# Kernel tuning notes

Measured on AMD Instinct MI355X. Metric: run time of the kernel, lower is better.

## Reference

```python
import jax, jax.numpy as jnp
import numpy as np

B, S, D, F_INT = 8, 1024, 1024, 4096
N_EDGES = 262144
NUM_REL = 2
LN_EPS = 1e-6


def setup_inputs() -> dict:
    key = jax.random.key(0)
    ks = jax.random.split(key, 10)
    N = B * S
    glorot_w = float(np.sqrt(6.0 / (D + F_INT)))
    glorot_r = float(np.sqrt(6.0 / (D + F_INT)))
    return {
        "hidden_states": jax.random.normal(ks[0], (B, S, D), dtype=jnp.float32),
        "weight": jax.random.uniform(ks[1], (NUM_REL, D, F_INT), jnp.float32, -glorot_w, glorot_w),
        "root": jax.random.uniform(ks[2], (D, F_INT), jnp.float32, -glorot_r, glorot_r),
        "bias": jnp.zeros((F_INT,), jnp.float32),
        "wo": jax.random.normal(ks[3], (F_INT, D), dtype=jnp.float32) * 0.02,
        "ln_gamma": jnp.ones((D,), jnp.float32),
        "ln_beta": jnp.zeros((D,), jnp.float32),
        "edge_index": jax.random.randint(ks[4], (2, N_EDGES), 0, N, dtype=jnp.int32),
        "edge_type": jax.random.randint(ks[5], (N_EDGES,), 0, NUM_REL, dtype=jnp.int32),
    }


def reference(hidden_states, weight, root, bias, wo, ln_gamma, ln_beta, edge_index, edge_type):
    Bz, Sq, Dm = hidden_states.shape
    N = Bz * Sq
    # LayerNorm
    mu = hidden_states.mean(-1, keepdims=True)
    var = jnp.mean((hidden_states - mu) ** 2, axis=-1, keepdims=True)
    norm_x = (hidden_states - mu) * jax.lax.rsqrt(var + LN_EPS) * ln_gamma + ln_beta
    x = norm_x.reshape(N, Dm)  # [N, D] node features

    src, dst = edge_index[0], edge_index[1]
    out = jnp.zeros((N, weight.shape[2]), dtype=x.dtype)
    # RGCNConv: per-relation masked gather -> scatter-mean -> matmul
    for r in range(NUM_REL):
        mask = (edge_type == r)
        msg = jnp.where(mask[:, None], x[src], 0.0)          # [E, D]
        agg = jax.ops.segment_sum(msg, dst, num_segments=N)  # [N, D]
        cnt = jax.ops.segment_sum(mask.astype(x.dtype), dst, num_segments=N)
        h = agg / jnp.maximum(cnt, 1.0)[:, None]             # mean aggr (0 if no edges)
        out = out + h @ weight[r]
    out = out + x @ root + bias
    # relu -> wo -> residual (dropout = identity at eval)
    out = jax.nn.relu(out) @ wo
    return hidden_states + out.reshape(Bz, Sq, Dm)
```

## Files before the change

### kernel.cpp

```cpp
#include <hip/hip_runtime.h>


typedef unsigned short u16;
typedef unsigned int   u32;
typedef __attribute__((ext_vector_type(8))) short bf16x8;
typedef __attribute__((ext_vector_type(4))) float f32x4;
typedef __attribute__((ext_vector_type(2))) float f32x2;

#define E_NUM  262144
#define NNODE  8192
#define NBKT   (2 * NNODE)
#define DDIM   1024
#define FDIM   4096
#define KCAT   3072
#define LN_EPS 1e-6f

struct alignas(8) u16x4 { u16 x, y, z, w; };

__device__ __forceinline__ u16 f2bf(float f) {
  u32 u = __float_as_uint(f);
  u32 r = u + 0x7fffu + ((u >> 16) & 1u);
  return (u16)(r >> 16);
}
__device__ __forceinline__ float bf2f(u16 h) {
  return __uint_as_float(((u32)h) << 16);
}

__device__ __forceinline__ u32 enc_fp8_1(float f) {
  u32 u = __float_as_uint(f);
  u32 s = u >> 31;
  u32 mag = u & 0x7fffffffu;
  mag = mag + 0x7ffffu + ((mag >> 20) & 1u);
  if (mag > 0x43e00000u) mag = 0x43e00000u;
  u32 e = mag >> 23;
  return (e <= 120u) ? 0u
                     : ((s << 7) | ((e - 120u) << 3) | ((mag >> 20) & 7u));
}

__device__ __forceinline__ u32 pack4_fp8(float a, float b, float c, float d) {
#if __has_builtin(__builtin_amdgcn_cvt_pk_fp8_f32)
  int v = 0;
  v = __builtin_amdgcn_cvt_pk_fp8_f32(a, b, v, false);
  v = __builtin_amdgcn_cvt_pk_fp8_f32(c, d, v, true);
  return (u32)v;
#else
  return enc_fp8_1(a) | (enc_fp8_1(b) << 8) | (enc_fp8_1(c) << 16) |
         (enc_fp8_1(d) << 24);
#endif
}

__device__ __forceinline__ float dec_fp8_1(u32 b) {
  u32 e = (b >> 3) & 15u;
  u32 f = ((b & 0x80u) << 24) | ((e + 120u) << 23) | ((b & 7u) << 20);
  return e ? __uint_as_float(f) : 0.0f;
}

__device__ __forceinline__ void acc4_fp8(float* a, u32 q) {
#if __has_builtin(__builtin_amdgcn_cvt_pk_f32_fp8)
  f32x2 p0 = __builtin_amdgcn_cvt_pk_f32_fp8((int)q, false);
  f32x2 p1 = __builtin_amdgcn_cvt_pk_f32_fp8((int)q, true);
  a[0] += p0.x; a[1] += p0.y; a[2] += p1.x; a[3] += p1.y;
#else
  a[0] += dec_fp8_1(q);       a[1] += dec_fp8_1(q >> 8);
  a[2] += dec_fp8_1(q >> 16); a[3] += dec_fp8_1(q >> 24);
#endif
}

#define GLD16(gp, lp)                                              \
  __builtin_amdgcn_global_load_lds(                                \
      (__attribute__((address_space(1))) u32*)(gp),                \
      (__attribute__((address_space(3))) u32*)(lp), 16, 0, 0)

__global__ void ln_kernel(const float* __restrict__ hs,
                          const float* __restrict__ gamma,
                          const float* __restrict__ beta,
                          u16* __restrict__ hcat,
                          u32* __restrict__ xq) {
  const int row = blockIdx.x;
  const int tid = threadIdx.x;
  const float4 v = ((const float4*)(hs + (size_t)row * DDIM))[tid];

  __shared__ float r1[256], r2[256];
  r1[tid] = v.x + v.y + v.z + v.w;
  r2[tid] = v.x * v.x + v.y * v.y + v.z * v.z + v.w * v.w;
  __syncthreads();
  for (int st = 128; st > 0; st >>= 1) {
    if (tid < st) { r1[tid] += r1[tid + st]; r2[tid] += r2[tid + st]; }
    __syncthreads();
  }
  const float mean = r1[0] * (1.0f / DDIM);
  const float var  = r2[0] * (1.0f / DDIM) - mean * mean;
  const float rs   = rsqrtf(var + LN_EPS);

  const int base = tid * 4;
  const float4 g = *(const float4*)(gamma + base);
  const float4 b = *(const float4*)(beta + base);
  const float o0 = (v.x - mean) * rs * g.x + b.x;
  const float o1 = (v.y - mean) * rs * g.y + b.y;
  const float o2 = (v.z - mean) * rs * g.z + b.z;
  const float o3 = (v.w - mean) * rs * g.w + b.w;
  u16x4 o;
  o.x = f2bf(o0); o.y = f2bf(o1); o.z = f2bf(o2); o.w = f2bf(o3);
  *(u16x4*)(hcat + (size_t)row * KCAT + 2048 + base) = o;
  xq[row * 256 + tid] = pack4_fp8(o0, o1, o2, o3);
}

__global__ void cvt_transpose(const float* __restrict__ srcA,
                              const float* __restrict__ srcB,
                              int splitK, int K, int N,
                              u16* __restrict__ dst) {
  __shared__ float tile[32][33];
  const int n0 = blockIdx.x * 32, k0 = blockIdx.y * 32;
  const int tx = threadIdx.x, ty = threadIdx.y;
  for (int i = ty; i < 32; i += 8) {
    const int k = k0 + i;
    const float v = (k < splitK) ? srcA[(size_t)k * N + n0 + tx]
                                 : srcB[(size_t)(k - splitK) * N + n0 + tx];
    tile[i][tx] = v;
  }
  __syncthreads();
  for (int i = ty; i < 32; i += 8) {
    dst[(size_t)(n0 + i) * K + k0 + tx] = f2bf(tile[tx][i]);
  }
}

__global__ void count_kernel(const int* __restrict__ edge_index,
                             const int* __restrict__ edge_type,
                             int* __restrict__ cnt) {
  const int e = blockIdx.x * 256 + threadIdx.x;
  const int d = edge_index[E_NUM + e];
  const int r = edge_type[e];
  atomicAdd(&cnt[r * NNODE + d], 1);
}

__global__ __launch_bounds__(1024) void scan_kernel(const int* __restrict__ cnt,
                                                    int* __restrict__ off,
                                                    int* __restrict__ cursor) {
  __shared__ int partial[1024];
  const int tid  = threadIdx.x;
  const int base = tid * 16;
  int local[16];
  int s = 0;
#pragma unroll
  for (int i = 0; i < 16; ++i) { local[i] = s; s += cnt[base + i]; }
  partial[tid] = s;
  __syncthreads();
  for (int st = 1; st < 1024; st <<= 1) {
    const int v = (tid >= st) ? partial[tid - st] : 0;
    __syncthreads();
    partial[tid] += v;
    __syncthreads();
  }
  const int pre = (tid == 0) ? 0 : partial[tid - 1];
#pragma unroll
  for (int i = 0; i < 16; ++i) {
    const int o = pre + local[i];
    off[base + i]    = o;
    cursor[base + i] = o;
  }
}

__global__ void fill_kernel(const int* __restrict__ edge_index,
                            const int* __restrict__ edge_type,
                            int* __restrict__ cursor,
                            int* __restrict__ bucket_src) {
  const int e = blockIdx.x * 256 + threadIdx.x;
  const int s = edge_index[e];
  const int d = edge_index[E_NUM + e];
  const int r = edge_type[e];
  const int pos = atomicAdd(&cursor[r * NNODE + d], 1);
  bucket_src[pos] = s;
}

__global__ __launch_bounds__(256) void aggregate_kernel(
    const int* __restrict__ cnt, const int* __restrict__ off,
    const int* __restrict__ bucket_src, const u32* __restrict__ xq,
    u16* __restrict__ hcat) {
  const int b    = blockIdx.x;
  const int r    = b >> 13;
  const int node = b & (NNODE - 1);
  const int tid  = threadIdx.x;
  const int g    = tid >> 6;
  const int c    = tid & 63;
  const int n     = cnt[b];
  const int start = off[b];

  __shared__ int   ids[256];
  __shared__ float red[3 * 1024];
  float a[16] = {};

  for (int c0 = 0; c0 < n; c0 += 256) {
    const int m = min(n - c0, 256);
    __syncthreads();
    if (tid < m) ids[tid] = bucket_src[start + c0 + tid];
    __syncthreads();
    int j = g;
    for (; j + 4 < m; j += 8) {
      const int s0 = ids[j], s1 = ids[j + 4];
      const uint4 x0 = *(const uint4*)(xq + s0 * 256 + c * 4);
      const uint4 x1 = *(const uint4*)(xq + s1 * 256 + c * 4);
      acc4_fp8(a + 0,  x0.x); acc4_fp8(a + 4,  x0.y);
      acc4_fp8(a + 8,  x0.z); acc4_fp8(a + 12, x0.w);
      acc4_fp8(a + 0,  x1.x); acc4_fp8(a + 4,  x1.y);
      acc4_fp8(a + 8,  x1.z); acc4_fp8(a + 12, x1.w);
    }
    for (; j < m; j += 4) {
      const int s0 = ids[j];
      const uint4 x0 = *(const uint4*)(xq + s0 * 256 + c * 4);
      acc4_fp8(a + 0,  x0.x); acc4_fp8(a + 4,  x0.y);
      acc4_fp8(a + 8,  x0.z); acc4_fp8(a + 12, x0.w);
    }
  }

  if (g != 0) {
    float* d = red + (g - 1) * 1024 + c * 16;
#pragma unroll
    for (int i = 0; i < 4; ++i)
      *(float4*)(d + i * 4) = make_float4(a[i*4+0], a[i*4+1], a[i*4+2], a[i*4+3]);
  }
  __syncthreads();
  if (g == 0) {
#pragma unroll
    for (int k = 0; k < 3; ++k) {
      const float* d = red + k * 1024 + c * 16;
#pragma unroll
      for (int i = 0; i < 16; ++i) a[i] += d[i];
    }
    const float inv = 1.0f / fmaxf((float)n, 1.0f);
    uint4 o0, o1;
    o0.x = (u32)f2bf(a[0] * inv)  | ((u32)f2bf(a[1] * inv)  << 16);
    o0.y = (u32)f2bf(a[2] * inv)  | ((u32)f2bf(a[3] * inv)  << 16);
    o0.z = (u32)f2bf(a[4] * inv)  | ((u32)f2bf(a[5] * inv)  << 16);
    o0.w = (u32)f2bf(a[6] * inv)  | ((u32)f2bf(a[7] * inv)  << 16);
    o1.x = (u32)f2bf(a[8] * inv)  | ((u32)f2bf(a[9] * inv)  << 16);
    o1.y = (u32)f2bf(a[10] * inv) | ((u32)f2bf(a[11] * inv) << 16);
    o1.z = (u32)f2bf(a[12] * inv) | ((u32)f2bf(a[13] * inv) << 16);
    o1.w = (u32)f2bf(a[14] * inv) | ((u32)f2bf(a[15] * inv) << 16);
    u16* dp = hcat + (size_t)node * KCAT + (size_t)r * DDIM + c * 16;
    *(uint4*)(dp)     = o0;
    *(uint4*)(dp + 8) = o1;
  }
}


#define MF16(a, b, c) __builtin_amdgcn_mfma_f32_16x16x32_bf16(a, b, c, 0, 0, 0)

#define STAGE_A(t, p, b)                                                   \
  { GLD16(gA0 + (size_t)(t) * 64 + (size_t)(p) * KP,                       \
          &sA[b][(p) * 8192 + lofs0]);                                     \
    GLD16(gA1 + (size_t)(t) * 64 + (size_t)(p) * KP,                       \
          &sA[b][(p) * 8192 + lofs1]); }

#define STAGE_B(t, p, b)                                                   \
  { GLD16(gB0 + (size_t)(t) * 64 + (size_t)(p) * KP,                       \
          &sB[b][(p) * 8192 + lofs0]);                                     \
    GLD16(gB1 + (size_t)(t) * 64 + (size_t)(p) * KP,                       \
          &sB[b][(p) * 8192 + lofs1]); }

#define BVLOAD(b)                                                          \
  { const bf16x8* pB_ = (const bf16x8*)sB[b];                              \
    bv[0][0] = pB_[brow80 + sega0]; bv[0][1] = pB_[brow80 + sega1];        \
    bv[1][0] = pB_[brow81 + sega0]; bv[1][1] = pB_[brow81 + sega1];        \
    bv[2][0] = pB_[brow82 + sega0]; bv[2][1] = pB_[brow82 + sega1];        \
    bv[3][0] = pB_[brow83 + sega0]; bv[3][1] = pB_[brow83 + sega1]; }

#define NOWAIT ((void)0)
#define NOSTAGE ((void)0)
#define VM4 asm volatile("s_waitcnt vmcnt(4)" ::: "memory")
#define VM0 asm volatile("s_waitcnt vmcnt(0)" ::: "memory")

#define PHASE(Q, BUFI, STAGE, ENDW)                                        \
  { const bf16x8* pA_ = (const bf16x8*)sA[BUFI];                           \
    bf16x8 a00 = pA_[arow8[2 * (Q)] + sega0];                              \
    bf16x8 a01 = pA_[arow8[2 * (Q)] + sega1];                              \
    bf16x8 a10 = pA_[arow8[2 * (Q) + 1] + sega0];                          \
    bf16x8 a11 = pA_[arow8[2 * (Q) + 1] + sega1];                          \
    STAGE;                                                                 \
    __builtin_amdgcn_s_barrier();                                          \
    asm volatile("s_waitcnt lgkmcnt(0)" ::: "memory");                     \
    __builtin_amdgcn_s_setprio(1);                                         \
    _Pragma("unroll")                                                      \
    for (int ni = 0; ni < 4; ++ni) {                                       \
      acc[2 * (Q)][ni]     = MF16(a00, bv[ni][0], acc[2 * (Q)][ni]);       \
      acc[2 * (Q)][ni]     = MF16(a01, bv[ni][1], acc[2 * (Q)][ni]);       \
      acc[2 * (Q) + 1][ni] = MF16(a10, bv[ni][0], acc[2 * (Q) + 1][ni]);   \
      acc[2 * (Q) + 1][ni] = MF16(a11, bv[ni][1], acc[2 * (Q) + 1][ni]);   \
    }                                                                      \
    __builtin_amdgcn_s_setprio(0);                                         \
    ENDW;                                                                  \
    __builtin_amdgcn_s_barrier(); }

__global__ __launch_bounds__(512) void gemm1_kernel(
    const u16* __restrict__ A, const u16* __restrict__ Bt,
    const float* __restrict__ bias, u16* __restrict__ obf) {
  const int K = KCAT, N = FDIM;
  const int NT = K / 64;
  const size_t KP = (size_t)128 * K;
  __shared__ __align__(16) u16 sA[2][16384];
  __shared__ __align__(16) u16 sB[2][16384];

  const int tid  = threadIdx.x;
  const int lane = tid & 63;
  const int wave = tid >> 6;
  const int wr = wave >> 2, wc = wave & 3;
  const int lr = lane & 15, quad = lane >> 4;

  const int bid = blockIdx.x;
  const int swz = (bid & 7) * 64 + (bid >> 3);
  const int bm = (swz >> 4) * 256;
  const int bn = (swz & 15) * 256;

  int lofs0, lofs1;
  const u16 *gA0, *gA1, *gB0, *gB1;
  {
    const int s0 = tid,       r0 = s0 >> 3, g0 = (s0 & 7) ^ (r0 & 7);
    const int s1 = tid + 512, r1 = s1 >> 3, g1 = (s1 & 7) ^ (r1 & 7);
    gA0 = A  + (size_t)(bm + r0) * K + g0 * 8;
    gA1 = A  + (size_t)(bm + r1) * K + g1 * 8;
    gB0 = Bt + (size_t)(bn + r0) * K + g0 * 8;
    gB1 = Bt + (size_t)(bn + r1) * K + g1 * 8;
    lofs0 = s0 * 8; lofs1 = s1 * 8;
  }

  int arow8[8];
#pragma unroll
  for (int mi = 0; mi < 8; ++mi) arow8[mi] = (wr * 128 + mi * 16 + lr) * 8;
  const int brow80 = (wc * 64 +  0 + lr) * 8;
  const int brow81 = (wc * 64 + 16 + lr) * 8;
  const int brow82 = (wc * 64 + 32 + lr) * 8;
  const int brow83 = (wc * 64 + 48 + lr) * 8;
  const int sega0 = quad ^ (lr & 7);
  const int sega1 = (4 + quad) ^ (lr & 7);

  f32x4 acc[8][4] = {};
  bf16x8 bv[4][2];

  STAGE_B(0, 0, 0) STAGE_B(0, 1, 0)
  STAGE_A(0, 0, 0) STAGE_A(0, 1, 0)
  STAGE_B(1, 0, 1) STAGE_B(1, 1, 1)
  asm volatile("s_waitcnt vmcnt(4)" ::: "memory");
  __builtin_amdgcn_s_barrier();

  for (int tt = 0; tt < NT - 2; tt += 2) {
    PHASE(0, 0, BVLOAD(0); STAGE_A(tt + 1, 0, 1), NOWAIT)
    PHASE(1, 0, STAGE_A(tt + 1, 1, 1), NOWAIT)
    PHASE(2, 0, STAGE_B(tt + 2, 0, 0), NOWAIT)
    PHASE(3, 0, STAGE_B(tt + 2, 1, 0), VM4)
    PHASE(0, 1, BVLOAD(1); STAGE_A(tt + 2, 0, 0), NOWAIT)
    PHASE(1, 1, STAGE_A(tt + 2, 1, 0), NOWAIT)
    PHASE(2, 1, STAGE_B(tt + 3, 0, 1), NOWAIT)
    PHASE(3, 1, STAGE_B(tt + 3, 1, 1), VM4)
  }
  PHASE(0, 0, BVLOAD(0); STAGE_A(NT - 1, 0, 1), NOWAIT)
  PHASE(1, 0, STAGE_A(NT - 1, 1, 1), NOWAIT)
  PHASE(2, 0, NOSTAGE, NOWAIT)
  PHASE(3, 0, NOSTAGE, VM0)
  PHASE(0, 1, BVLOAD(1), NOWAIT)
  PHASE(1, 1, NOSTAGE, NOWAIT)
  PHASE(2, 1, NOSTAGE, NOWAIT)
  PHASE(3, 1, NOSTAGE, NOWAIT)

#pragma unroll
  for (int mi = 0; mi < 8; ++mi) {
#pragma unroll
    for (int ni = 0; ni < 4; ++ni) {
      const int col  = bn + wc * 64 + ni * 16 + lr;
      const int row0 = bm + wr * 128 + mi * 16 + quad * 4;
      const float bb = bias[col];
#pragma unroll
      for (int r = 0; r < 4; ++r) {
        float v = acc[mi][ni][r] + bb;
        v = fmaxf(v, 0.0f);
        obf[(size_t)(row0 + r) * N + col] = f2bf(v);
      }
    }
  }
}

__global__ __launch_bounds__(256) void gemm2_kernel(
    const u16* __restrict__ A, const u16* __restrict__ Bt,
    const float* __restrict__ resid, float* __restrict__ out) {
  const int K = FDIM, N = DDIM;
  __shared__ __align__(16) u16 sA[64 * 64];
  __shared__ __align__(16) u16 sB[128 * 64];
  const int tid  = threadIdx.x;
  const int lane = tid & 63;
  const int wave = tid >> 6;
  const int bm = blockIdx.x * 64;
  const int bn = blockIdx.y * 128;
  const int wm = (wave >> 1) * 32;
  const int wn = (wave & 1) * 64;
  const int lr   = lane & 15;
  const int quad = lane >> 4;

  f32x4 acc[2][4] = {};

  const u16* gA[2]; u16* lA[2];
#pragma unroll
  for (int i = 0; i < 2; ++i) {
    const int s   = tid + 256 * i;
    const int row = s >> 3;
    const int seg = (s & 7) ^ (row & 7);
    gA[i] = A + (size_t)(bm + row) * K + seg * 8;
    lA[i] = sA + s * 8;
  }
  const u16* gB[4]; u16* lB[4];
#pragma unroll
  for (int i = 0; i < 4; ++i) {
    const int s   = tid + 256 * i;
    const int row = s >> 3;
    const int seg = (s & 7) ^ (row & 7);
    gB[i] = Bt + (size_t)(bn + row) * K + seg * 8;
    lB[i] = sB + s * 8;
  }

  int ai[2][2], bi[4][2];
#pragma unroll
  for (int h = 0; h < 2; ++h) {
#pragma unroll
    for (int mi = 0; mi < 2; ++mi) {
      const int ra = wm + mi * 16 + lr;
      ai[mi][h] = ra * 8 + ((h * 4 + quad) ^ (ra & 7));
    }
#pragma unroll
    for (int ni = 0; ni < 4; ++ni) {
      const int rb = wn + ni * 16 + lr;
      bi[ni][h] = rb * 8 + ((h * 4 + quad) ^ (rb & 7));
    }
  }

  for (int k0 = 0; k0 < K; k0 += 64) {
#pragma unroll
    for (int i = 0; i < 2; ++i) GLD16(gA[i] + k0, lA[i]);
#pragma unroll
    for (int i = 0; i < 4; ++i) GLD16(gB[i] + k0, lB[i]);
    __syncthreads();

    const bf16x8* pA = (const bf16x8*)sA;
    const bf16x8* pB = (const bf16x8*)sB;
#pragma unroll
    for (int h = 0; h < 2; ++h) {
      bf16x8 av[2], bv[4];
#pragma unroll
      for (int mi = 0; mi < 2; ++mi) av[mi] = pA[ai[mi][h]];
#pragma unroll
      for (int ni = 0; ni < 4; ++ni) bv[ni] = pB[bi[ni][h]];
#pragma unroll
      for (int mi = 0; mi < 2; ++mi)
#pragma unroll
        for (int ni = 0; ni < 4; ++ni)
          acc[mi][ni] = __builtin_amdgcn_mfma_f32_16x16x32_bf16(
              av[mi], bv[ni], acc[mi][ni], 0, 0, 0);
    }
    __syncthreads();
  }

#pragma unroll
  for (int mi = 0; mi < 2; ++mi) {
#pragma unroll
    for (int ni = 0; ni < 4; ++ni) {
      const int col  = bn + wn + ni * 16 + lr;
      const int row0 = bm + wm + mi * 16 + quad * 4;
#pragma unroll
      for (int r = 0; r < 4; ++r) {
        const size_t idx = (size_t)(row0 + r) * N + col;
        out[idx] = resid[idx] + acc[mi][ni][r];
      }
    }
  }
}

extern "C" void kernel_launch(void* const* d_in, const int* in_sizes, int n_in,
                              void* d_out, int out_size, void* d_ws, size_t ws_size,
                              hipStream_t stream) {
  const float* hs     = (const float*)d_in[0];
  const float* weight = (const float*)d_in[1];
  const float* root   = (const float*)d_in[2];
  const float* bias   = (const float*)d_in[3];
  const float* wo     = (const float*)d_in[4];
  const float* gamma  = (const float*)d_in[5];
  const float* beta   = (const float*)d_in[6];
  const int* edge_index = (const int*)d_in[7];
  const int* edge_type  = (const int*)d_in[8];
  float* out = (float*)d_out;

  char* ws = (char*)d_ws;
  u16*   hcat       = (u16*)(ws + 0);
  u16*   WcatT      = (u16*)(ws + 50331648);
  u16*   woT        = (u16*)(ws + 75497472);
  u16*   out1       = (u16*)(ws + 83886080);
  int*   bucket_src = (int*)(ws + 83886080);
  int*   cnt        = (int*)(ws + 84934656);
  int*   off        = (int*)(ws + 85000192);
  int*   cursor     = (int*)(ws + 85065728);
  u32*   xq         = (u32*)(ws + 85131264);

  (void)hipMemsetAsync(cnt, 0, 65536, stream);

  ln_kernel<<<NNODE, 256, 0, stream>>>(hs, gamma, beta, hcat, xq);

  cvt_transpose<<<dim3(FDIM / 32, KCAT / 32), dim3(32, 8), 0, stream>>>(
      weight, root, 2048, KCAT, FDIM, WcatT);
  cvt_transpose<<<dim3(DDIM / 32, FDIM / 32), dim3(32, 8), 0, stream>>>(
      wo, wo, FDIM, FDIM, DDIM, woT);

  count_kernel<<<E_NUM / 256, 256, 0, stream>>>(edge_index, edge_type, cnt);
  scan_kernel<<<1, 1024, 0, stream>>>(cnt, off, cursor);
  fill_kernel<<<E_NUM / 256, 256, 0, stream>>>(edge_index, edge_type, cursor, bucket_src);
  aggregate_kernel<<<NBKT, 256, 0, stream>>>(cnt, off, bucket_src, xq, hcat);

  gemm1_kernel<<<512, 512, 0, stream>>>(hcat, WcatT, bias, out1);

  gemm2_kernel<<<dim3(8192 / 64, DDIM / 128), 256, 0, stream>>>(
      out1, woT, hs, out);
}
```

Measured before the change: 501.5 us.

## Rewrite gemm2 with double-buffered pipelined phases and larger 256x128 tiles

Restructures the second GEMM (relu output times wo) to reuse the gemm1-style software pipeline. Global-to-LDS loads are double-buffered and interleaved with MFMA phases using vmcnt waits and setprio. Each block is now 512 threads on a 256x128 tile with a swizzled block index for L2 locality. The old version synchronised twice per K-step with no overlap. The trade-off is a much smaller grid (256 blocks) and higher LDS and register use per block.

```diff
diff --git a/kernel.cpp b/kernel.cpp
--- a/kernel.cpp
+++ b/kernel.cpp
@@ -267,6 +267,7 @@
 #define NOWAIT ((void)0)
 #define NOSTAGE ((void)0)
 #define VM4 asm volatile("s_waitcnt vmcnt(4)" ::: "memory")
+#define VM2 asm volatile("s_waitcnt vmcnt(2)" ::: "memory")
 #define VM0 asm volatile("s_waitcnt vmcnt(0)" ::: "memory")
 
 #define PHASE(Q, BUFI, STAGE, ENDW)                                        \
@@ -377,90 +378,74 @@
   }
 }
 
-__global__ __launch_bounds__(256) void gemm2_kernel(
+__global__ __launch_bounds__(512) void gemm2_kernel(
     const u16* __restrict__ A, const u16* __restrict__ Bt,
     const float* __restrict__ resid, float* __restrict__ out) {
   const int K = FDIM, N = DDIM;
-  __shared__ __align__(16) u16 sA[64 * 64];
-  __shared__ __align__(16) u16 sB[128 * 64];
+  const int NT = K / 64;
+  const size_t KP = (size_t)128 * K;
+  __shared__ __align__(16) u16 sA[2][16384];
+  __shared__ __align__(16) u16 sB[2][8192];
+
   const int tid  = threadIdx.x;
   const int lane = tid & 63;
   const int wave = tid >> 6;
-  const int bm = blockIdx.x * 64;
-  const int bn = blockIdx.y * 128;
-  const int wm = (wave >> 1) * 32;
-  const int wn = (wave & 1) * 64;
-  const int lr   = lane & 15;
-  const int quad = lane >> 4;
-
-  f32x4 acc[2][4] = {};
-
-  const u16* gA[2]; u16* lA[2];
-#pragma unroll
-  for (int i = 0; i < 2; ++i) {
-    const int s   = tid + 256 * i;
-    const int row = s >> 3;
-    const int seg = (s & 7) ^ (row & 7);
-    gA[i] = A + (size_t)(bm + row) * K + seg * 8;
-    lA[i] = sA + s * 8;
-  }
-  const u16* gB[4]; u16* lB[4];
-#pragma unroll
-  for (int i = 0; i < 4; ++i) {
-    const int s   = tid + 256 * i;
-    const int row = s >> 3;
-    const int seg = (s & 7) ^ (row & 7);
-    gB[i] = Bt + (size_t)(bn + row) * K + seg * 8;
-    lB[i] = sB + s * 8;
-  }
-
-  int ai[2][2], bi[4][2];
-#pragma unroll
-  for (int h = 0; h < 2; ++h) {
-#pragma unroll
-    for (int mi = 0; mi < 2; ++mi) {
-      const int ra = wm + mi * 16 + lr;
-      ai[mi][h] = ra * 8 + ((h * 4 + quad) ^ (ra & 7));
-    }
+  const int wr = wave >> 1, wc = wave & 1;
+  const int lr = lane & 15, quad = lane >> 4;
+
+  const int bid = blockIdx.x;
+  const int swz = (bid & 7) * 32 + (bid >> 3);
+  const int bm = (swz >> 3) * 256;
+  const int bn = (swz & 7) * 128;
+
+  int lofs0, lofs1;
+  const u16 *gA0, *gA1, *gB0, *gB1;
+  {
+    const int s0 = tid,       r0 = s0 >> 3, g0 = (s0 & 7) ^ (r0 & 7);
+    const int s1 = tid + 512, r1 = s1 >> 3, g1 = (s1 & 7) ^ (r1 & 7);
+    gA0 = A  + (size_t)(bm + r0) * K + g0 * 8;
+    gA1 = A  + (size_t)(bm + r1) * K + g1 * 8;
+    gB0 = Bt + (size_t)(bn + r0) * K + g0 * 8;
+    gB1 = Bt + (size_t)(bn + r1) * K + g1 * 8;
+    lofs0 = s0 * 8; lofs1 = s1 * 8;
+  }
+
+  int arow8[4];
+#pragma unroll
+  for (int mi = 0; mi < 4; ++mi) arow8[mi] = (wr * 64 + mi * 16 + lr) * 8;
+  const int brow80 = (wc * 64 +  0 + lr) * 8;
+  const int brow81 = (wc * 64 + 16 + lr) * 8;
+  const int brow82 = (wc * 64 + 32 + lr) * 8;
+  const int brow83 = (wc * 64 + 48 + lr) * 8;
+  const int sega0 = quad ^ (lr & 7);
+  const int sega1 = (4 + quad) ^ (lr & 7);
+
+  f32x4 acc[4][4] = {};
+  bf16x8 bv[4][2];
+
+  STAGE_B(0, 0, 0)
+  STAGE_A(0, 0, 0) STAGE_A(0, 1, 0)
+  STAGE_B(1, 0, 1)
+  asm volatile("s_waitcnt vmcnt(2)" ::: "memory");
+  __builtin_amdgcn_s_barrier();
+
+  for (int tt = 0; tt < NT - 2; tt += 2) {
+    PHASE(0, 0, BVLOAD(0); STAGE_A(tt + 1, 0, 1), NOWAIT)
+    PHASE(1, 0, STAGE_A(tt + 1, 1, 1); STAGE_B(tt + 2, 0, 0), VM2)
+    PHASE(0, 1, BVLOAD(1); STAGE_A(tt + 2, 0, 0), NOWAIT)
+    PHASE(1, 1, STAGE_A(tt + 2, 1, 0); STAGE_B(tt + 3, 0, 1), VM2)
+  }
+  PHASE(0, 0, BVLOAD(0); STAGE_A(NT - 1, 0, 1), NOWAIT)
+  PHASE(1, 0, STAGE_A(NT - 1, 1, 1), VM0)
+  PHASE(0, 1, BVLOAD(1), NOWAIT)
+  PHASE(1, 1, NOSTAGE, NOWAIT)
+
+#pragma unroll
+  for (int mi = 0; mi < 4; ++mi) {
 #pragma unroll
     for (int ni = 0; ni < 4; ++ni) {
-      const int rb = wn + ni * 16 + lr;
-      bi[ni][h] = rb * 8 + ((h * 4 + quad) ^ (rb & 7));
-    }
-  }
-
-  for (int k0 = 0; k0 < K; k0 += 64) {
-#pragma unroll
-    for (int i = 0; i < 2; ++i) GLD16(gA[i] + k0, lA[i]);
-#pragma unroll
-    for (int i = 0; i < 4; ++i) GLD16(gB[i] + k0, lB[i]);
-    __syncthreads();
-
-    const bf16x8* pA = (const bf16x8*)sA;
-    const bf16x8* pB = (const bf16x8*)sB;
-#pragma unroll
-    for (int h = 0; h < 2; ++h) {
-      bf16x8 av[2], bv[4];
-#pragma unroll
-      for (int mi = 0; mi < 2; ++mi) av[mi] = pA[ai[mi][h]];
-#pragma unroll
-      for (int ni = 0; ni < 4; ++ni) bv[ni] = pB[bi[ni][h]];
-#pragma unroll
-      for (int mi = 0; mi < 2; ++mi)
-#pragma unroll
-        for (int ni = 0; ni < 4; ++ni)
-          acc[mi][ni] = __builtin_amdgcn_mfma_f32_16x16x32_bf16(
-              av[mi], bv[ni], acc[mi][ni], 0, 0, 0);
-    }
-    __syncthreads();
-  }
-
-#pragma unroll
-  for (int mi = 0; mi < 2; ++mi) {
-#pragma unroll
-    for (int ni = 0; ni < 4; ++ni) {
-      const int col  = bn + wn + ni * 16 + lr;
-      const int row0 = bm + wm + mi * 16 + quad * 4;
+      const int col  = bn + wc * 64 + ni * 16 + lr;
+      const int row0 = bm + wr * 64 + mi * 16 + quad * 4;
 #pragma unroll
       for (int r = 0; r < 4; ++r) {
         const size_t idx = (size_t)(row0 + r) * N + col;
@@ -511,6 +496,5 @@
 
   gemm1_kernel<<<512, 512, 0, stream>>>(hcat, WcatT, bias, out1);
 
-  gemm2_kernel<<<dim3(8192 / 64, DDIM / 128), 256, 0, stream>>>(
-      out1, woT, hs, out);
-}
+  gemm2_kernel<<<256, 512, 0, stream>>>(out1, woT, hs, out);
+}
```

Result: faster. 474.5 us (-5.4%).
